# Optimization experiments

Measured on AMD Instinct MI355X. Metric: run time of the kernel, lower is better.

## Reference

```python
import jax, jax.numpy as jnp
import numpy as np

INPUT_DIM = 16
NUM_MFS = 4
NUM_RULES = 1024
NUM_CLASSES = 10
BATCH = 4096


def setup_inputs() -> dict:
    key = jax.random.key(0)
    k1, k2, k3, k4, k5 = jax.random.split(key, 5)
    x = jax.random.normal(k1, (BATCH, INPUT_DIM), dtype=jnp.float32)
    centers = jax.random.normal(k2, (INPUT_DIM, NUM_MFS), dtype=jnp.float32)
    # widths must be positive (used as std of gaussian)
    widths = jax.random.uniform(k3, (INPUT_DIM, NUM_MFS), dtype=jnp.float32, minval=0.2, maxval=1.2)
    consequents = jax.random.normal(k4, (NUM_RULES, INPUT_DIM + 1, NUM_CLASSES), dtype=jnp.float32)
    rule_idx = jax.random.randint(k5, (INPUT_DIM, NUM_RULES), 0, NUM_MFS, dtype=jnp.int32)
    return {"x": x, "centers": centers, "widths": widths,
            "consequents": consequents, "rule_idx": rule_idx}


def reference(x, centers, widths, consequents, rule_idx):
    B, D = x.shape
    # Gaussian membership functions: [B, D, M]
    mfs = jnp.exp(-((x[:, :, None] - centers[None]) ** 2) / (2.0 * widths[None] ** 2) + 1e-9)
    # Gather rule-specific memberships: [B, D, R]
    d_idx = jnp.arange(D)[:, None]  # [D, 1] broadcasts with rule_idx [D, R]
    rule_mfs = mfs[:, d_idx, rule_idx]
    # Firing strengths (product over input dims) and normalization: [B, R]
    firing = jnp.prod(rule_mfs, axis=1)
    norm_fs = firing / (jnp.sum(firing, axis=1, keepdims=True) + 1e-9)
    # Extended input with bias column: [B, D+1]
    x_ext = jnp.concatenate([x, jnp.ones((B, 1), dtype=x.dtype)], axis=1)
    # phi = norm_fs[:, :, None] * x_ext[:, None, :]; y = phi_flat @ beta_flat
    # expressed as a single contraction (same math, phi is detached w.r.t. x_ext)
    y_hat = jnp.einsum('br,bi,ric->bc', norm_fs, jax.lax.stop_gradient(x_ext), consequents)
    return y_hat, norm_fs, x_ext
```

## Files before the change

kernel.cpp:

```cpp
#include <hip/hip_runtime.h>

#define B 4096
#define D 16
#define R 1024
#define NC 10
#define IC 170
#define NT 11
#define NP 176
#define KSPLIT 8
#define RPB (R / KSPLIT)
#define BT 64
#define BSTR 136
#define GSP 180

typedef __attribute__((ext_vector_type(8))) short short8;
typedef __attribute__((ext_vector_type(4))) float f32x4;

__device__ __forceinline__ unsigned short f2bf(float f) {
    unsigned u = __float_as_uint(f);
    return (unsigned short)((u + 0x7fffu + ((u >> 16) & 1u)) >> 16);
}

__global__ __launch_bounds__(256) void prep_kernel(
    const float* __restrict__ cons, unsigned short* __restrict__ Bsw,
    const int* __restrict__ rule_idx, unsigned* __restrict__ packed,
    float* __restrict__ out_y)
{
    const int bid = blockIdx.x, tid = threadIdx.x;
    if (bid < 704) {
        int t = bid * 256 + tid;
        int row = t >> 10;
        int k   = t & 1023;
        float v = (row < IC) ? cons[(size_t)k * IC + row] : 0.0f;
        Bsw[t] = f2bf(v);
    } else if (bid < 708) {
        int r = (bid - 704) * 256 + tid;
        unsigned bits = 0;
#pragma unroll
        for (int d = 0; d < D; ++d)
            bits |= (((unsigned)rule_idx[d * R + r]) & 3u) << (2 * d);
        packed[r] = bits;
    } else {
        out_y[(bid - 708) * 256 + tid] = 0.0f;
    }
}

__global__ __launch_bounds__(256) void firing_kernel(
    const float* __restrict__ x, const float* __restrict__ centers,
    const float* __restrict__ widths, const unsigned* __restrict__ packed,
    float* __restrict__ out_norm, float* __restrict__ out_xext)
{
    __shared__ float s_z2[8][16];
    __shared__ float s_z4[4 * 256];
    __shared__ float s_red[4];
    const int b = blockIdx.x, tid = threadIdx.x;
    const int lane = tid & 63, wv = tid >> 6;

    {
        int d = lane >> 2;
        float xv = x[b * D + d];
        float c = centers[lane], w = widths[lane];
        float diff = xv - c;
        float z = 1e-9f - diff * diff / (2.0f * w * w);

        if (tid < 17) out_xext[b * 17 + tid] = (tid < 16) ? x[b * D + tid] : 1.0f;

        if (wv < 2) {
            int p = tid >> 4, i = tid & 15;
            float za = __shfl(z, p * 8 + (i & 3), 64);
            float zb = __shfl(z, p * 8 + 4 + ((i >> 2) & 3), 64);
            s_z2[p][i] = za + zb;
        }
    }
    __syncthreads();
#pragma unroll
    for (int q = 0; q < 4; ++q)
        s_z4[q * 256 + tid] = s_z2[2 * q][tid & 15] + s_z2[2 * q + 1][(tid >> 4) & 15];
    __syncthreads();

    uint4 pw = *(const uint4*)&packed[4 * tid];
    unsigned wq[4] = {pw.x, pw.y, pw.z, pw.w};
    float f[4], lsum = 0.0f;
#pragma unroll
    for (int k = 0; k < 4; ++k) {
        unsigned wk = wq[k];
        float s = s_z4[wk & 255] + s_z4[256 + ((wk >> 8) & 255)]
                + s_z4[512 + ((wk >> 16) & 255)] + s_z4[768 + (wk >> 24)];
        f[k] = __expf(s);
        lsum += f[k];
    }
#pragma unroll
    for (int off = 1; off < 64; off <<= 1) lsum += __shfl_xor(lsum, off, 64);
    if (lane == 0) s_red[wv] = lsum;
    __syncthreads();
    const float inv = 1.0f / (s_red[0] + s_red[1] + s_red[2] + s_red[3] + 1e-9f);
    float4 o;
    o.x = f[0] * inv; o.y = f[1] * inv; o.z = f[2] * inv; o.w = f[3] * inv;
    *(float4*)&out_norm[(size_t)b * R + 4 * tid] = o;
}

__global__ __launch_bounds__(256, 2) void yhat_kernel(
    const float* __restrict__ norm, const unsigned short* __restrict__ Bsw,
    const float* __restrict__ x, float* __restrict__ out_y)
{
    __shared__ unsigned short Bs[NP * BSTR];
    __shared__ unsigned short As[BT * BSTR];
    __shared__ float xe[BT * 17];

    const int tid = threadIdx.x;
    const int mt = blockIdx.x & 63;
    const int ks = blockIdx.x >> 6;
    const int bl0 = mt * BT;
    const int kabs = ks * RPB;

    for (int t = tid; t < BT * 17; t += 256) {
        int bl = t / 17, i = t - bl * 17;
        xe[t] = (i < 16) ? x[(size_t)(bl0 + bl) * D + i] : 1.0f;
    }
    for (int t = tid; t < NP * 16; t += 256) {
        int row = t >> 4, seg = t & 15;
        *(short8*)&Bs[row * BSTR + seg * 8] =
            *(const short8*)&Bsw[row * R + kabs + seg * 8];
    }
    for (int t = tid; t < BT * 32; t += 256) {
        int row = t >> 5, c4 = t & 31;
        float4 v = *(const float4*)&norm[(size_t)(bl0 + row) * R + kabs + c4 * 4];
        ushort4 o;
        o.x = f2bf(v.x); o.y = f2bf(v.y); o.z = f2bf(v.z); o.w = f2bf(v.w);
        *(ushort4*)&As[row * BSTR + c4 * 4] = o;
    }
    __syncthreads();

    const int lane = tid & 63, wv = tid >> 6;
    const int m_ = lane & 15, q_ = lane >> 4;
    const int nt0 = wv * 3;
    const int ntn = (wv == 3) ? 2 : 3;

    f32x4 acc[4][3];
    const f32x4 zf = {0.f, 0.f, 0.f, 0.f};
#pragma unroll
    for (int mb = 0; mb < 4; ++mb)
#pragma unroll
        for (int j = 0; j < 3; ++j) acc[mb][j] = zf;

#pragma unroll
    for (int kh = 0; kh < 4; ++kh) {
        short8 a[4];
#pragma unroll
        for (int mb = 0; mb < 4; ++mb)
            a[mb] = *(const short8*)&As[(mb * 16 + m_) * BSTR + kh * 32 + q_ * 8];
#pragma unroll
        for (int j = 0; j < 3; ++j) {
            if (j < ntn) {
                short8 bfrag = *(const short8*)&Bs[((nt0 + j) * 16 + m_) * BSTR + kh * 32 + q_ * 8];
#pragma unroll
                for (int mb = 0; mb < 4; ++mb)
                    acc[mb][j] = __builtin_amdgcn_mfma_f32_16x16x32_bf16(a[mb], bfrag, acc[mb][j], 0, 0, 0);
            }
        }
    }

    __syncthreads();
    float* Gs = (float*)Bs;
#pragma unroll
    for (int j = 0; j < 3; ++j) {
        if (j < ntn) {
            int nt = nt0 + j;
#pragma unroll
            for (int mb = 0; mb < 4; ++mb)
#pragma unroll
                for (int r = 0; r < 4; ++r)
                    Gs[(mb * 16 + q_ * 4 + r) * GSP + nt * 16 + m_] = acc[mb][j][r];
        }
    }
    __syncthreads();
    for (int t = tid; t < BT * NC; t += 256) {
        int bl = t / NC, c = t - bl * NC;
        float y = 0.0f;
#pragma unroll
        for (int i = 0; i < 17; ++i)
            y += xe[bl * 17 + i] * Gs[bl * GSP + i * NC + c];
        atomicAdd(&out_y[(size_t)(bl0 + bl) * NC + c], y);
    }
}

extern "C" void kernel_launch(void* const* d_in, const int* in_sizes, int n_in,
                              void* d_out, int out_size, void* d_ws, size_t ws_size,
                              hipStream_t stream) {
    const float* x        = (const float*)d_in[0];
    const float* centers  = (const float*)d_in[1];
    const float* widths   = (const float*)d_in[2];
    const float* cons     = (const float*)d_in[3];
    const int*   rule_idx = (const int*)d_in[4];

    float* out      = (float*)d_out;
    float* out_y    = out;
    float* out_norm = out + (size_t)B * NC;
    float* out_xext = out + (size_t)B * NC + (size_t)B * R;

    unsigned* packed     = (unsigned*)d_ws;
    unsigned short* Bsw  = (unsigned short*)((char*)d_ws + 4096);

    prep_kernel<<<868, 256, 0, stream>>>(cons, Bsw, rule_idx, packed, out_y);
    firing_kernel<<<B, 256, 0, stream>>>(x, centers, widths, packed,
                                         out_norm, out_xext);
    yhat_kernel<<<(B / BT) * KSPLIT, 256, 0, stream>>>(out_norm, Bsw, x, out_y);
}
```

Measured before the change: 91.46 us.

## Fuse firing and y-hat kernels; compute log-firing sums via one-hot MFMA

Merges the firing-strength kernel and the split-K y-hat GEMM into one kernel per 16-row batch tile. Log-membership sums are computed with an MFMA against a one-hot rule-indicator matrix, using z split into hi/lo bf16 parts. The unnormalized firing values go straight into the consequent GEMM and normalization is applied at the end. This removes the round trip of norm through global memory, the zeroing pass and the atomics. In exchange it uses larger LDS with one block per CU, reads B fragments directly from global memory, and the bf16 hi/lo split may lose precision in the exponent sums.

```diff
diff --git a/kernel.cpp b/kernel.cpp
--- a/kernel.cpp
+++ b/kernel.cpp
@@ -7,11 +7,11 @@
 #define IC 170
 #define NT 11
 #define NP 176
-#define KSPLIT 8
-#define RPB (R / KSPLIT)
-#define BT 64
-#define BSTR 136
-#define GSP 180
+#define BT 16
+#define NBLK (B / BT)
+#define ZSTR 136
+#define FSTR 264
+#define GSP 178
 
 typedef __attribute__((ext_vector_type(8))) short short8;
 typedef __attribute__((ext_vector_type(4))) float f32x4;
@@ -23,8 +23,7 @@
 
 __global__ __launch_bounds__(256) void prep_kernel(
     const float* __restrict__ cons, unsigned short* __restrict__ Bsw,
-    const int* __restrict__ rule_idx, unsigned* __restrict__ packed,
-    float* __restrict__ out_y)
+    const int* __restrict__ rule_idx, unsigned short* __restrict__ Ind2)
 {
     const int bid = blockIdx.x, tid = threadIdx.x;
     if (bid < 704) {
@@ -33,154 +32,153 @@
         int k   = t & 1023;
         float v = (row < IC) ? cons[(size_t)k * IC + row] : 0.0f;
         Bsw[t] = f2bf(v);
-    } else if (bid < 708) {
+    } else {
         int r = (bid - 704) * 256 + tid;
-        unsigned bits = 0;
-#pragma unroll
-        for (int d = 0; d < D; ++d)
-            bits |= (((unsigned)rule_idx[d * R + r]) & 3u) << (2 * d);
-        packed[r] = bits;
-    } else {
-        out_y[(bid - 708) * 256 + tid] = 0.0f;
-    }
-}
-
-__global__ __launch_bounds__(256) void firing_kernel(
+#pragma unroll
+        for (int d = 0; d < D; ++d) {
+            int mi = rule_idx[d * R + r];
+            uint4 v;
+            v.x = (mi == 0) ? 0x3F803F80u : 0u;
+            v.y = (mi == 1) ? 0x3F803F80u : 0u;
+            v.z = (mi == 2) ? 0x3F803F80u : 0u;
+            v.w = (mi == 3) ? 0x3F803F80u : 0u;
+            *(uint4*)&Ind2[(size_t)r * 128 + d * 8] = v;
+        }
+    }
+}
+
+__global__ __launch_bounds__(256, 1) void fused_kernel(
     const float* __restrict__ x, const float* __restrict__ centers,
-    const float* __restrict__ widths, const unsigned* __restrict__ packed,
-    float* __restrict__ out_norm, float* __restrict__ out_xext)
+    const float* __restrict__ widths, const unsigned short* __restrict__ Ind2,
+    const unsigned short* __restrict__ Bsw,
+    float* __restrict__ out_y, float* __restrict__ out_norm,
+    float* __restrict__ out_xext)
 {
-    __shared__ float s_z2[8][16];
-    __shared__ float s_z4[4 * 256];
-    __shared__ float s_red[4];
-    const int b = blockIdx.x, tid = threadIdx.x;
+    __shared__ union U {
+        struct {
+            unsigned short Zs[BT * ZSTR];
+            unsigned short fAs[4][BT * FSTR];
+        } p1;
+        float Gs[4][BT * GSP];
+    } u;
+    __shared__ float xe[BT * 17];
+    __shared__ float s_red[4 * BT];
+
+    const int tid = threadIdx.x;
+    const int bl0 = blockIdx.x * BT;
     const int lane = tid & 63, wv = tid >> 6;
-
-    {
-        int d = lane >> 2;
-        float xv = x[b * D + d];
-        float c = centers[lane], w = widths[lane];
+    const int m_ = lane & 15, q_ = lane >> 4;
+
+    for (int t = tid; t < BT * 17; t += 256) {
+        int bl = t / 17, i = t - bl * 17;
+        float v = (i < 16) ? x[(size_t)(bl0 + bl) * D + i] : 1.0f;
+        xe[t] = v;
+        out_xext[(size_t)(bl0 + bl) * 17 + i] = v;
+    }
+    for (int p = tid; p < BT * 64; p += 256) {
+        int s = p >> 6, j = p & 63;
+        int d = j >> 2;
+        float xv = x[(size_t)(bl0 + s) * D + d];
+        float c = centers[j], w = widths[j];
         float diff = xv - c;
         float z = 1e-9f - diff * diff / (2.0f * w * w);
-
-        if (tid < 17) out_xext[b * 17 + tid] = (tid < 16) ? x[b * D + tid] : 1.0f;
-
-        if (wv < 2) {
-            int p = tid >> 4, i = tid & 15;
-            float za = __shfl(z, p * 8 + (i & 3), 64);
-            float zb = __shfl(z, p * 8 + 4 + ((i >> 2) & 3), 64);
-            s_z2[p][i] = za + zb;
-        }
-    }
-    __syncthreads();
-#pragma unroll
-    for (int q = 0; q < 4; ++q)
-        s_z4[q * 256 + tid] = s_z2[2 * q][tid & 15] + s_z2[2 * q + 1][(tid >> 4) & 15];
-    __syncthreads();
-
-    uint4 pw = *(const uint4*)&packed[4 * tid];
-    unsigned wq[4] = {pw.x, pw.y, pw.z, pw.w};
-    float f[4], lsum = 0.0f;
-#pragma unroll
-    for (int k = 0; k < 4; ++k) {
-        unsigned wk = wq[k];
-        float s = s_z4[wk & 255] + s_z4[256 + ((wk >> 8) & 255)]
-                + s_z4[512 + ((wk >> 16) & 255)] + s_z4[768 + (wk >> 24)];
-        f[k] = __expf(s);
-        lsum += f[k];
-    }
-#pragma unroll
-    for (int off = 1; off < 64; off <<= 1) lsum += __shfl_xor(lsum, off, 64);
-    if (lane == 0) s_red[wv] = lsum;
-    __syncthreads();
-    const float inv = 1.0f / (s_red[0] + s_red[1] + s_red[2] + s_red[3] + 1e-9f);
-    float4 o;
-    o.x = f[0] * inv; o.y = f[1] * inv; o.z = f[2] * inv; o.w = f[3] * inv;
-    *(float4*)&out_norm[(size_t)b * R + 4 * tid] = o;
-}
-
-__global__ __launch_bounds__(256, 2) void yhat_kernel(
-    const float* __restrict__ norm, const unsigned short* __restrict__ Bsw,
-    const float* __restrict__ x, float* __restrict__ out_y)
-{
-    __shared__ unsigned short Bs[NP * BSTR];
-    __shared__ unsigned short As[BT * BSTR];
-    __shared__ float xe[BT * 17];
-
-    const int tid = threadIdx.x;
-    const int mt = blockIdx.x & 63;
-    const int ks = blockIdx.x >> 6;
-    const int bl0 = mt * BT;
-    const int kabs = ks * RPB;
-
-    for (int t = tid; t < BT * 17; t += 256) {
-        int bl = t / 17, i = t - bl * 17;
-        xe[t] = (i < 16) ? x[(size_t)(bl0 + bl) * D + i] : 1.0f;
-    }
-    for (int t = tid; t < NP * 16; t += 256) {
-        int row = t >> 4, seg = t & 15;
-        *(short8*)&Bs[row * BSTR + seg * 8] =
-            *(const short8*)&Bsw[row * R + kabs + seg * 8];
-    }
-    for (int t = tid; t < BT * 32; t += 256) {
-        int row = t >> 5, c4 = t & 31;
-        float4 v = *(const float4*)&norm[(size_t)(bl0 + row) * R + kabs + c4 * 4];
-        ushort4 o;
-        o.x = f2bf(v.x); o.y = f2bf(v.y); o.z = f2bf(v.z); o.w = f2bf(v.w);
-        *(ushort4*)&As[row * BSTR + c4 * 4] = o;
-    }
-    __syncthreads();
-
-    const int lane = tid & 63, wv = tid >> 6;
-    const int m_ = lane & 15, q_ = lane >> 4;
-    const int nt0 = wv * 3;
-    const int ntn = (wv == 3) ? 2 : 3;
-
-    f32x4 acc[4][3];
+        unsigned short zh = f2bf(z);
+        float zhf = __uint_as_float((unsigned)zh << 16);
+        unsigned short zl = f2bf(z - zhf);
+        *(unsigned*)&u.p1.Zs[s * ZSTR + 2 * j] = (unsigned)zh | ((unsigned)zl << 16);
+    }
+    __syncthreads();
+
+    short8 za[4];
+#pragma unroll
+    for (int kh = 0; kh < 4; ++kh)
+        za[kh] = *(const short8*)&u.p1.Zs[m_ * ZSTR + kh * 32 + q_ * 8];
+
+    f32x4 acc1[16];
     const f32x4 zf = {0.f, 0.f, 0.f, 0.f};
 #pragma unroll
-    for (int mb = 0; mb < 4; ++mb)
-#pragma unroll
-        for (int j = 0; j < 3; ++j) acc[mb][j] = zf;
+    for (int nt = 0; nt < 16; ++nt) acc1[nt] = zf;
 
 #pragma unroll
     for (int kh = 0; kh < 4; ++kh) {
-        short8 a[4];
-#pragma unroll
-        for (int mb = 0; mb < 4; ++mb)
-            a[mb] = *(const short8*)&As[(mb * 16 + m_) * BSTR + kh * 32 + q_ * 8];
-#pragma unroll
-        for (int j = 0; j < 3; ++j) {
-            if (j < ntn) {
-                short8 bfrag = *(const short8*)&Bs[((nt0 + j) * 16 + m_) * BSTR + kh * 32 + q_ * 8];
-#pragma unroll
-                for (int mb = 0; mb < 4; ++mb)
-                    acc[mb][j] = __builtin_amdgcn_mfma_f32_16x16x32_bf16(a[mb], bfrag, acc[mb][j], 0, 0, 0);
-            }
-        }
-    }
-
-    __syncthreads();
-    float* Gs = (float*)Bs;
-#pragma unroll
-    for (int j = 0; j < 3; ++j) {
-        if (j < ntn) {
-            int nt = nt0 + j;
-#pragma unroll
-            for (int mb = 0; mb < 4; ++mb)
-#pragma unroll
-                for (int r = 0; r < 4; ++r)
-                    Gs[(mb * 16 + q_ * 4 + r) * GSP + nt * 16 + m_] = acc[mb][j][r];
-        }
-    }
-    __syncthreads();
-    for (int t = tid; t < BT * NC; t += 256) {
-        int bl = t / NC, c = t - bl * NC;
-        float y = 0.0f;
-#pragma unroll
-        for (int i = 0; i < 17; ++i)
-            y += xe[bl * 17 + i] * Gs[bl * GSP + i * NC + c];
-        atomicAdd(&out_y[(size_t)(bl0 + bl) * NC + c], y);
+#pragma unroll
+        for (int nt = 0; nt < 16; ++nt) {
+            int rule = (wv * 16 + nt) * 16 + m_;
+            short8 bf = *(const short8*)&Ind2[(size_t)rule * 128 + kh * 32 + q_ * 8];
+            acc1[nt] = __builtin_amdgcn_mfma_f32_16x16x32_bf16(za[kh], bf, acc1[nt], 0, 0, 0);
+        }
+    }
+
+    float f[16][4];
+    float part[4] = {0.f, 0.f, 0.f, 0.f};
+#pragma unroll
+    for (int nt = 0; nt < 16; ++nt) {
+#pragma unroll
+        for (int r = 0; r < 4; ++r) {
+            float v = __expf(acc1[nt][r]);
+            f[nt][r] = v;
+            part[r] += v;
+            u.p1.fAs[wv][(q_ * 4 + r) * FSTR + nt * 16 + m_] = f2bf(v);
+        }
+    }
+#pragma unroll
+    for (int off = 1; off < 16; off <<= 1)
+#pragma unroll
+        for (int r = 0; r < 4; ++r) part[r] += __shfl_xor(part[r], off, 64);
+    if (m_ == 0) {
+#pragma unroll
+        for (int r = 0; r < 4; ++r) s_red[wv * BT + q_ * 4 + r] = part[r];
+    }
+    __syncthreads();
+
+    f32x4 acc2[11];
+#pragma unroll
+    for (int j = 0; j < 11; ++j) acc2[j] = zf;
+
+#pragma unroll
+    for (int kh = 0; kh < 8; ++kh) {
+        short8 a = *(const short8*)&u.p1.fAs[wv][m_ * FSTR + kh * 32 + q_ * 8];
+#pragma unroll
+        for (int j = 0; j < 11; ++j) {
+            int col = j * 16 + m_;
+            short8 bf = *(const short8*)&Bsw[(size_t)col * R + wv * 256 + kh * 32 + q_ * 8];
+            acc2[j] = __builtin_amdgcn_mfma_f32_16x16x32_bf16(a, bf, acc2[j], 0, 0, 0);
+        }
+    }
+    __syncthreads();
+
+    float invr[4];
+#pragma unroll
+    for (int r = 0; r < 4; ++r) {
+        int s = q_ * 4 + r;
+        invr[r] = 1.0f / (s_red[s] + s_red[16 + s] + s_red[32 + s] + s_red[48 + s] + 1e-9f);
+    }
+#pragma unroll
+    for (int nt = 0; nt < 16; ++nt) {
+        int rule = (wv * 16 + nt) * 16 + m_;
+#pragma unroll
+        for (int r = 0; r < 4; ++r)
+            out_norm[(size_t)(bl0 + q_ * 4 + r) * R + rule] = f[nt][r] * invr[r];
+    }
+
+#pragma unroll
+    for (int j = 0; j < 11; ++j)
+#pragma unroll
+        for (int r = 0; r < 4; ++r)
+            u.Gs[wv][(q_ * 4 + r) * GSP + j * 16 + m_] = acc2[j][r];
+    __syncthreads();
+
+    if (tid < BT * NC) {
+        int bl = tid / NC, c = tid - bl * NC;
+        float inv = 1.0f / (s_red[bl] + s_red[16 + bl] + s_red[32 + bl] + s_red[48 + bl] + 1e-9f);
+        float y = 0.f;
+#pragma unroll
+        for (int i = 0; i < 17; ++i) {
+            int gi = bl * GSP + i * NC + c;
+            float g = u.Gs[0][gi] + u.Gs[1][gi] + u.Gs[2][gi] + u.Gs[3][gi];
+            y += xe[bl * 17 + i] * g;
+        }
+        out_y[(size_t)(bl0 + bl) * NC + c] = y * inv;
     }
 }
 
@@ -198,11 +196,10 @@
     float* out_norm = out + (size_t)B * NC;
     float* out_xext = out + (size_t)B * NC + (size_t)B * R;
 
-    unsigned* packed     = (unsigned*)d_ws;
-    unsigned short* Bsw  = (unsigned short*)((char*)d_ws + 4096);
-
-    prep_kernel<<<868, 256, 0, stream>>>(cons, Bsw, rule_idx, packed, out_y);
-    firing_kernel<<<B, 256, 0, stream>>>(x, centers, widths, packed,
-                                         out_norm, out_xext);
-    yhat_kernel<<<(B / BT) * KSPLIT, 256, 0, stream>>>(out_norm, Bsw, x, out_y);
-}
+    unsigned short* Bsw  = (unsigned short*)d_ws;
+    unsigned short* Ind2 = (unsigned short*)((char*)d_ws + 360448);
+
+    prep_kernel<<<708, 256, 0, stream>>>(cons, Bsw, rule_idx, Ind2);
+    fused_kernel<<<NBLK, 256, 0, stream>>>(x, centers, widths, Ind2, Bsw,
+                                           out_y, out_norm, out_xext);
+}
```

Measured after the change: 102.3 us. 11.9% more time.
